# Kernel optimization log

Hardware: AMD Instinct MI355X
Metric: run time of the kernel (lower is better)

Reference implementation:

```python
import jax, jax.numpy as jnp
import numpy as np

B, IN, H, Z = 2048, 1024, 1024, 256


def setup_inputs() -> dict:
    key = jax.random.key(0)
    ks = jax.random.split(key, 17)
    s = 1.0 / np.sqrt(H)  # matches reset_parameters uniform(-stdv, stdv)
    u = lambda k, shape: jax.random.uniform(k, shape, minval=-s, maxval=s, dtype=jnp.float32)
    return {
        'src_x': jax.random.normal(ks[0], (B, IN), dtype=jnp.float32),
        'h': jax.random.normal(ks[1], (B, H), dtype=jnp.float32),
        'c': jax.random.normal(ks[2], (B, H), dtype=jnp.float32),
        'src_meta': jax.random.normal(ks[3], (B, Z), dtype=jnp.float32),
        'zh_w': u(ks[4], (4 * Z, Z)),
        'zh_b': u(ks[5], (4 * Z,)),
        'zx_w': u(ks[6], (4 * Z, Z)),
        'zx_b': u(ks[7], (4 * Z,)),
        'zb_w': u(ks[8], (4 * Z, Z)),
        'dh_w': u(ks[9], (4, H, Z)),
        'dx_w': u(ks[10], (4, H, Z)),
        'db_w': u(ks[11], (4, H, Z)),
        'db_b': u(ks[12], (4, H)),
        'w_h': u(ks[13], (4, H, H)),
        'w_x': u(ks[14], (4, H, IN)),
        'ln_w': u(ks[15], (4, H)),
        'ln_b': u(ks[16], (4, H)),
    }


def reference(src_x, h, c, src_meta, zh_w, zh_b, zx_w, zx_b, zb_w,
              dh_w, dx_w, db_w, db_b, w_h, w_x, ln_w, ln_b):
    b = src_x.shape[0]
    # hypernetwork projections, reshaped to [B, 4 gates, Z]
    zh = (src_meta @ zh_w.T + zh_b).reshape(b, 4, -1)
    zx = (src_meta @ zx_w.T + zx_b).reshape(b, 4, -1)
    zb = (src_meta @ zb_w.T).reshape(b, 4, -1)
    # per-gate scaling vectors d_h, d_x and bias d_b: [B, 4, H]
    d_h = jnp.einsum('bgz,ghz->bgh', zh, dh_w)
    d_x = jnp.einsum('bgz,ghz->bgh', zx, dx_w)
    d_b = jnp.einsum('bgz,ghz->bgh', zb, db_w) + db_b[None]
    # main LSTM matmuls: [B, 4, H]
    wh = jnp.einsum('ghj,bj->bgh', w_h, h)
    wx = jnp.einsum('ghj,bj->bgh', w_x, src_x)
    y = d_h * wh + d_x * wx + d_b
    # per-gate LayerNorm over hidden dim (eps = 1e-5, torch default)
    mu = jnp.mean(y, axis=-1, keepdims=True)
    var = jnp.var(y, axis=-1, keepdims=True)
    yn = (y - mu) * jax.lax.rsqrt(var + 1e-5) * ln_w[None] + ln_b[None]
    i, f, g, o = yn[:, 0], yn[:, 1], yn[:, 2], yn[:, 3]
    c_next = jax.nn.sigmoid(f) * c + jax.nn.sigmoid(i) * jnp.tanh(g)
    h_next = jax.nn.sigmoid(o) * jnp.tanh(c_next)
    return (h_next, c_next)
```

## Files before the change

kernel.cpp:

```cpp
#include <hip/hip_runtime.h>

typedef __attribute__((ext_vector_type(4))) float f32x4;
typedef __attribute__((ext_vector_type(16))) float f32x16;
typedef __attribute__((ext_vector_type(8))) short bf16x8;

#define DEVFN static __device__ __forceinline__

DEVFN unsigned short f2bf(float f) {
  union { float f; unsigned u; } x; x.f = f;
  unsigned r = x.u + 0x7fffu + ((x.u >> 16) & 1u);
  return (unsigned short)(r >> 16);
}
DEVFN float bf2f(unsigned short u) {
  union { unsigned u; float f; } x; x.u = ((unsigned)u) << 16;
  return x.f;
}

DEVFN void gload_lds16(const unsigned short* g, unsigned short* l) {
  __builtin_amdgcn_global_load_lds(
      (const __attribute__((address_space(1))) unsigned int*)g,
      (__attribute__((address_space(3))) unsigned int*)l, 16, 0, 0);
}

#define NSEG 8
struct SegTable {
  const float* src[NSEG];
  unsigned short* dst[NSEG];
  int chunks[NSEG];
};

__global__ __launch_bounds__(256) void cast_f32_bf16(SegTable st) {
  int c = blockIdx.x;
  int s = 0;
  while (c >= st.chunks[s]) { c -= st.chunks[s]; ++s; }
  const float* src = st.src[s] + (long)c * 4096;
  unsigned short* dst = st.dst[s] + (long)c * 4096;
  const int t = threadIdx.x;
#pragma unroll
  for (int i = 0; i < 4; ++i) {
    float4 v = *(const float4*)(src + t * 4 + i * 1024);
    ushort4 o;
    o.x = f2bf(v.x); o.y = f2bf(v.y); o.z = f2bf(v.z); o.w = f2bf(v.w);
    *(ushort4*)(dst + t * 4 + i * 1024) = o;
  }
}

__global__ __launch_bounds__(256) void tcast_z(
    const float* __restrict__ zh_w, const float* __restrict__ zx_w,
    const float* __restrict__ zb_w, unsigned short* __restrict__ WzT) {
  const int zz = blockIdx.z;
  const int t = zz >> 2, g = zz & 3;
  const float* src =
      (t == 0 ? zh_w : (t == 1 ? zx_w : zb_w)) + (long)g * 65536;
  unsigned short* dst = WzT + (long)zz * 65536;
  const int j0 = blockIdx.x * 64, k0 = blockIdx.y * 64;
  __shared__ float T[64][65];
  const int tid = threadIdx.x;
  const int jr = tid >> 2, kc = (tid & 3) * 16;
#pragma unroll
  for (int i = 0; i < 4; ++i) {
    float4 v = *(const float4*)(src + (long)(j0 + jr) * 256 + k0 + kc + i * 4);
    T[jr][kc + i * 4 + 0] = v.x;
    T[jr][kc + i * 4 + 1] = v.y;
    T[jr][kc + i * 4 + 2] = v.z;
    T[jr][kc + i * 4 + 3] = v.w;
  }
  __syncthreads();
  const int kr = tid >> 2, jc = (tid & 3) * 16;
  unsigned short tmp[16];
#pragma unroll
  for (int i = 0; i < 16; ++i) tmp[i] = f2bf(T[jc + i][kr]);
  *(bf16x8*)(dst + (long)(k0 + kr) * 256 + j0 + jc) = *(bf16x8*)&tmp[0];
  *(bf16x8*)(dst + (long)(k0 + kr) * 256 + j0 + jc + 8) = *(bf16x8*)&tmp[8];
}

__global__ __launch_bounds__(256) void fbias_kernel(
    const float* __restrict__ zh_b, const float* __restrict__ zx_b,
    const float* __restrict__ db_b, const float* __restrict__ dh_w,
    const float* __restrict__ dx_w, float* __restrict__ F) {
  if (blockIdx.x >= 128) {
    const int idx = (blockIdx.x - 128) * 1024 + threadIdx.x * 4;
    *(float4*)(F + 8192 + idx) = *(const float4*)(db_b + idx);
    return;
  }
  const int wgid = blockIdx.x * 4 + (threadIdx.x >> 6);
  const int lane = threadIdx.x & 63;
  const int t = wgid >> 8, g = (wgid >> 6) & 3, hbase = (wgid & 63) * 16;
  const float* zb = (t == 0 ? zh_b : zx_b) + g * 256;
  const float* dw = (t == 0 ? dh_w : dx_w) + (long)g * 262144;
  float4 zv = *(const float4*)(zb + lane * 4);
#pragma unroll
  for (int i = 0; i < 16; ++i) {
    const int h = hbase + i;
    float4 wv = *(const float4*)(dw + (long)h * 256 + lane * 4);
    float s = zv.x * wv.x + zv.y * wv.y + zv.z * wv.z + zv.w * wv.w;
#pragma unroll
    for (int off = 32; off; off >>= 1) s += __shfl_down(s, off);
    if (lane == 0) F[(t * 4 + g) * 1024 + h] = s;
  }
}

DEVFN void gemm128_body(const unsigned short* __restrict__ A,
                        const unsigned short* __restrict__ W,
                        unsigned short* __restrict__ C,
                        const float* __restrict__ bias,
                        int lda, int ldb, int ldc, int K,
                        int bx, int by,
                        unsigned short* As, unsigned short* Bs) {
  const int m0 = by * 128, n0 = bx * 128;
  const int tid = threadIdx.x;
  const int lane = tid & 63, wid = tid >> 6;
  const int wr = wid >> 1, wc = wid & 1;

  const int srow = tid >> 2, scol = (tid & 3) * 8;
  const unsigned short* Ag0 = A + (long)(m0 + srow) * lda + scol;
  const unsigned short* Ag1 = A + (long)(m0 + 64 + srow) * lda + scol;
  const unsigned short* Wg0 = W + (long)(n0 + srow) * ldb + scol;
  const unsigned short* Wg1 = W + (long)(n0 + 64 + srow) * ldb + scol;
  unsigned short* As0 = &As[tid * 8];
  unsigned short* As1 = &As[2048 + tid * 8];
  unsigned short* Bs0 = &Bs[tid * 8];
  unsigned short* Bs1 = &Bs[2048 + tid * 8];

  const int r = lane & 15, q = lane >> 4;

  f32x4 acc[4][4];
#pragma unroll
  for (int m = 0; m < 4; ++m)
#pragma unroll
    for (int n = 0; n < 4; ++n) acc[m][n] = (f32x4)0.f;

  for (int k0 = 0; k0 < K; k0 += 32) {
    gload_lds16(Ag0 + k0, As0);
    gload_lds16(Ag1 + k0, As1);
    gload_lds16(Wg0 + k0, Bs0);
    gload_lds16(Wg1 + k0, Bs1);
    __syncthreads();

    bf16x8 af[4], bfr[4];
#pragma unroll
    for (int m = 0; m < 4; ++m)
      af[m] = *(const bf16x8*)&As[(wr * 64 + m * 16 + r) * 32 + q * 8];
#pragma unroll
    for (int n = 0; n < 4; ++n)
      bfr[n] = *(const bf16x8*)&Bs[(wc * 64 + n * 16 + r) * 32 + q * 8];
#pragma unroll
    for (int m = 0; m < 4; ++m)
#pragma unroll
      for (int n = 0; n < 4; ++n)
        acc[m][n] = __builtin_amdgcn_mfma_f32_16x16x32_bf16(af[m], bfr[n],
                                                            acc[m][n], 0, 0, 0);
    __syncthreads();
  }

#pragma unroll
  for (int m = 0; m < 4; ++m) {
    const int row = m0 + wr * 64 + m * 16 + q * 4;
#pragma unroll
    for (int n = 0; n < 4; ++n) {
      const int col = n0 + wc * 64 + n * 16 + r;
      float bv = bias ? bias[col] : 0.f;
#pragma unroll
      for (int j = 0; j < 4; ++j) {
        float v = acc[m][n][j] + bv;
        C[(long)(row + j) * ldc + col] = f2bf(v);
      }
    }
  }
}

__global__ __launch_bounds__(256) void gemm_e(
    const unsigned short* __restrict__ Wd, const unsigned short* __restrict__ WzT,
    unsigned short* __restrict__ E) {
  __shared__ __align__(16) unsigned short As[4096];
  __shared__ __align__(16) unsigned short Bs[4096];
  const int zz = blockIdx.z;
  gemm128_body(Wd + (long)zz * 262144, WzT + (long)zz * 65536,
               E + (long)zz * 262144, nullptr,
               256, 256, 256, 256, blockIdx.x, blockIdx.y, As, Bs);
}

__global__ __launch_bounds__(256) void gemm_d(
    const unsigned short* __restrict__ meta_bf, const unsigned short* __restrict__ E,
    unsigned short* __restrict__ dall, const float* __restrict__ F) {
  __shared__ __align__(16) unsigned short As[4096];
  __shared__ __align__(16) unsigned short Bs[4096];
  const int zz = blockIdx.z;
  unsigned short* C = dall + (long)(zz >> 2) * 8388608 + (zz & 3) * 1024;
  gemm128_body(meta_bf, E + (long)zz * 262144, C, F + zz * 1024,
               256, 256, 4096, 256, blockIdx.x, blockIdx.y, As, Bs);
}

__global__ __launch_bounds__(512, 2) void gemm256_whx(
    const unsigned short* __restrict__ Aall,
    const unsigned short* __restrict__ Ball,
    unsigned short* __restrict__ Call) {
  __shared__ __align__(16) unsigned short As[2][2][8192];
  __shared__ __align__(16) unsigned short Bs[2][2][8192];

  const int bid = blockIdx.x;
  const int swz = (bid & 7) * 32 + (bid >> 3);
  const int z = swz >> 7;
  const int rr = swz & 127;
  const int sb = rr >> 5, wq = rr & 31;
  const int my = (sb & 1) * 4 + (wq >> 3);
  const int nx = (sb >> 1) * 8 + (wq & 7);

  const unsigned short* Ag = Aall + (long)z * 2097152 + (long)my * 262144;
  const unsigned short* Bg = Ball + (long)z * 4194304 + (long)nx * 262144;
  unsigned short* Cg = Call + (long)z * 8388608 + (long)my * 1048576 + nx * 256;

  const int tid = threadIdx.x;
  const int lane = tid & 63, wid = tid >> 6;
  const int wm = wid >> 2, wn = wid & 3;
  const int l31 = lane & 31, l5 = lane >> 5;
  const int sw = l31 & 7;

  const int srow = tid >> 3, sslot = tid & 7;
  const int gcol = (sslot ^ (srow & 7)) * 8;
  const unsigned short* AgS = Ag + (long)srow * 1024 + gcol;
  const unsigned short* BgS = Bg + (long)srow * 1024 + gcol;

  auto stageA = [&](int buf, int half, int kt) {
    const unsigned short* s = AgS + half * 131072 + kt * 64;
    unsigned short* d = &As[buf][half][tid * 8];
    gload_lds16(s, d);
    gload_lds16(s + 65536, d + 4096);
  };
  auto stageB = [&](int buf, int half, int kt) {
    const unsigned short* s = BgS + half * 131072 + kt * 64;
    unsigned short* d = &Bs[buf][half][tid * 8];
    gload_lds16(s, d);
    gload_lds16(s + 65536, d + 4096);
  };

  int koff[4];
#pragma unroll
  for (int ks = 0; ks < 4; ++ks) koff[ks] = ((ks * 2 + l5) ^ sw) * 8;

  const int bhalf = wn >> 1;
  int brow[2];
#pragma unroll
  for (int nt = 0; nt < 2; ++nt) brow[nt] = ((wn & 1) * 64 + nt * 32 + l31) * 64;
  int arow[4];
#pragma unroll
  for (int mt = 0; mt < 4; ++mt) arow[mt] = (mt * 32 + l31) * 64;

  f32x16 acc[4][2];
#pragma unroll
  for (int m = 0; m < 4; ++m)
#pragma unroll
    for (int n = 0; n < 2; ++n) acc[m][n] = (f32x16)0.f;

  stageA(0, 0, 0); stageB(0, 0, 0); stageA(0, 1, 0); stageB(0, 1, 0);
  stageA(1, 0, 1); stageB(1, 0, 1);
  asm volatile("s_waitcnt vmcnt(4)" ::: "memory");
  __builtin_amdgcn_s_barrier();

#pragma unroll 2
  for (int T = 0; T < 16; ++T) {
    const int buf = T & 1, nb = buf ^ 1;

    if (T < 15) { stageA(nb, 1, T + 1); stageB(nb, 1, T + 1); }

    bf16x8 bfg[2][4], af[2][4];
    const unsigned short* Ab = &As[buf][wm][0];
    {
      const unsigned short* Bb = &Bs[buf][bhalf][0];
#pragma unroll
      for (int nt = 0; nt < 2; ++nt)
#pragma unroll
        for (int ks = 0; ks < 4; ++ks)
          bfg[nt][ks] = *(const bf16x8*)(Bb + brow[nt] + koff[ks]);
#pragma unroll
      for (int m2 = 0; m2 < 2; ++m2)
#pragma unroll
        for (int ks = 0; ks < 4; ++ks)
          af[m2][ks] = *(const bf16x8*)(Ab + arow[m2] + koff[ks]);
    }

    __builtin_amdgcn_s_setprio(1);
#pragma unroll
    for (int m2 = 0; m2 < 2; ++m2)
#pragma unroll
      for (int nt = 0; nt < 2; ++nt)
#pragma unroll
        for (int ks = 0; ks < 4; ++ks)
          acc[m2][nt] = __builtin_amdgcn_mfma_f32_32x32x16_bf16(
              af[m2][ks], bfg[nt][ks], acc[m2][nt], 0, 0, 0);
    __builtin_amdgcn_s_setprio(0);

#pragma unroll
    for (int m2 = 0; m2 < 2; ++m2)
#pragma unroll
      for (int ks = 0; ks < 4; ++ks)
        af[m2][ks] = *(const bf16x8*)(Ab + arow[2 + m2] + koff[ks]);

    asm volatile("s_waitcnt lgkmcnt(0)" ::: "memory");
    __builtin_amdgcn_sched_barrier(0);
    __builtin_amdgcn_s_barrier();

    if (T < 14) { stageA(buf, 0, T + 2); stageB(buf, 0, T + 2); }

    __builtin_amdgcn_s_setprio(1);
#pragma unroll
    for (int m2 = 0; m2 < 2; ++m2)
#pragma unroll
      for (int nt = 0; nt < 2; ++nt)
#pragma unroll
        for (int ks = 0; ks < 4; ++ks)
          acc[2 + m2][nt] = __builtin_amdgcn_mfma_f32_32x32x16_bf16(
              af[m2][ks], bfg[nt][ks], acc[2 + m2][nt], 0, 0, 0);
    __builtin_amdgcn_s_setprio(0);

    if (T < 14) {
      asm volatile("s_waitcnt vmcnt(4)" ::: "memory");
      __builtin_amdgcn_s_barrier();
    } else if (T == 14) {
      asm volatile("s_waitcnt vmcnt(0)" ::: "memory");
      __builtin_amdgcn_s_barrier();
    }
  }

#pragma unroll
  for (int mt = 0; mt < 4; ++mt) {
#pragma unroll
    for (int nt = 0; nt < 2; ++nt) {
      const int rb = wm * 128 + mt * 32 + 4 * l5;
      const int cb = wn * 64 + nt * 32 + l31;
#pragma unroll
      for (int reg = 0; reg < 16; ++reg) {
        const int row = rb + (reg & 3) + 8 * (reg >> 2);
        Cg[(long)row * 4096 + cb] = f2bf(acc[mt][nt][reg]);
      }
    }
  }
}

DEVFN void ld4bf(const unsigned short* p, float* o) {
  ushort4 v = *(const ushort4*)p;
  o[0] = bf2f(v.x); o[1] = bf2f(v.y); o[2] = bf2f(v.z); o[3] = bf2f(v.w);
}

__global__ __launch_bounds__(256) void epilogue_kernel(
    const unsigned short* __restrict__ d_all,
    const unsigned short* __restrict__ whx,
    const float* __restrict__ c_in,
    const float* __restrict__ ln_w, const float* __restrict__ ln_b,
    float* __restrict__ out) {
  const long b = blockIdx.x;
  const int t = threadIdx.x;
  const int lane = t & 63, wid = t >> 6;

  const unsigned short* dh = d_all + b * 4096;
  const unsigned short* dx = d_all + 8388608L + b * 4096;
  const unsigned short* db = d_all + 16777216L + b * 4096;
  const unsigned short* wh = whx + b * 4096;
  const unsigned short* wx = whx + 8388608L + b * 4096;

  __shared__ float redS[4][4], redQ[4][4];
  float y[4][4];

#pragma unroll
  for (int g = 0; g < 4; ++g) {
    const int base = g * 1024 + t * 4;
    float fdh[4], fdx[4], fdb[4], fwh[4], fwx[4];
    ld4bf(dh + base, fdh);
    ld4bf(dx + base, fdx);
    ld4bf(db + base, fdb);
    ld4bf(wh + base, fwh);
    ld4bf(wx + base, fwx);
    float s = 0.f, sq = 0.f;
#pragma unroll
    for (int j = 0; j < 4; ++j) {
      float v = fdh[j] * fwh[j] + fdx[j] * fwx[j] + fdb[j];
      y[g][j] = v;
      s += v;
      sq += v * v;
    }
#pragma unroll
    for (int off = 32; off; off >>= 1) {
      s += __shfl_down(s, off);
      sq += __shfl_down(sq, off);
    }
    if (lane == 0) { redS[g][wid] = s; redQ[g][wid] = sq; }
  }
  __syncthreads();

  float yn[4][4];
#pragma unroll
  for (int g = 0; g < 4; ++g) {
    float S = redS[g][0] + redS[g][1] + redS[g][2] + redS[g][3];
    float SQ = redQ[g][0] + redQ[g][1] + redQ[g][2] + redQ[g][3];
    float mu = S * (1.f / 1024.f);
    float var = SQ * (1.f / 1024.f) - mu * mu;
    float rs = rsqrtf(var + 1e-5f);
    const int base = g * 1024 + t * 4;
    float4 lw = *(const float4*)(ln_w + base);
    float4 lb = *(const float4*)(ln_b + base);
    yn[g][0] = (y[g][0] - mu) * rs * lw.x + lb.x;
    yn[g][1] = (y[g][1] - mu) * rs * lw.y + lb.y;
    yn[g][2] = (y[g][2] - mu) * rs * lw.z + lb.z;
    yn[g][3] = (y[g][3] - mu) * rs * lw.w + lb.w;
  }

  float4 cp = *(const float4*)(c_in + b * 1024 + t * 4);
  float cin[4] = {cp.x, cp.y, cp.z, cp.w};
  float hn[4], cn[4];
#pragma unroll
  for (int j = 0; j < 4; ++j) {
    float ii = yn[0][j], ff = yn[1][j], gg = yn[2][j], oo = yn[3][j];
    float si = 1.f / (1.f + expf(-ii));
    float sf = 1.f / (1.f + expf(-ff));
    float so = 1.f / (1.f + expf(-oo));
    float cnj = sf * cin[j] + si * tanhf(gg);
    cn[j] = cnj;
    hn[j] = so * tanhf(cnj);
  }
  float4 ho = {hn[0], hn[1], hn[2], hn[3]};
  float4 co = {cn[0], cn[1], cn[2], cn[3]};
  *(float4*)(out + b * 1024 + t * 4) = ho;
  *(float4*)(out + 2097152L + b * 1024 + t * 4) = co;
}

extern "C" void kernel_launch(void* const* d_in, const int* in_sizes, int n_in,
                              void* d_out, int out_size, void* d_ws,
                              size_t ws_size, hipStream_t stream) {
  const float* src_x = (const float*)d_in[0];
  const float* h_in  = (const float*)d_in[1];
  const float* c_in  = (const float*)d_in[2];
  const float* meta  = (const float*)d_in[3];
  const float* zh_w  = (const float*)d_in[4];
  const float* zh_b  = (const float*)d_in[5];
  const float* zx_w  = (const float*)d_in[6];
  const float* zx_b  = (const float*)d_in[7];
  const float* zb_w  = (const float*)d_in[8];
  const float* dh_w  = (const float*)d_in[9];
  const float* dx_w  = (const float*)d_in[10];
  const float* db_w  = (const float*)d_in[11];
  const float* db_b  = (const float*)d_in[12];
  const float* w_h   = (const float*)d_in[13];
  const float* w_x   = (const float*)d_in[14];
  const float* ln_w  = (const float*)d_in[15];
  const float* ln_b  = (const float*)d_in[16];

  char* ws = (char*)d_ws;
  unsigned short* h_bf    = (unsigned short*)(ws + 0);
  unsigned short* x_bf    = (unsigned short*)(ws + 4194304);
  unsigned short* meta_bf = (unsigned short*)(ws + 8388608);
  unsigned short* Wh      = (unsigned short*)(ws + 9437184);
  unsigned short* Wx      = (unsigned short*)(ws + 17825792);
  unsigned short* Wd      = (unsigned short*)(ws + 26214400);
  unsigned short* WzT     = (unsigned short*)(ws + 32505856);
  unsigned short* E       = (unsigned short*)(ws + 34078720);
  float*          F       = (float*)(ws + 40370176);
  unsigned short* dall    = (unsigned short*)(ws + 40419328);
  unsigned short* whx     = (unsigned short*)(ws + 90750976);
  if (ws_size < 124305408) return;

  SegTable st;
  int i = 0, total = 0;
  auto add = [&](const float* s, unsigned short* d, int n) {
    st.src[i] = s; st.dst[i] = d; st.chunks[i] = n / 4096;
    total += n / 4096; ++i;
  };
  add(h_in, h_bf, 2048 * 1024);
  add(src_x, x_bf, 2048 * 1024);
  add(meta, meta_bf, 2048 * 256);
  add(w_h, Wh, 4096 * 1024);
  add(w_x, Wx, 4096 * 1024);
  add(dh_w, Wd, 4 * 1024 * 256);
  add(dx_w, Wd + 1048576, 4 * 1024 * 256);
  add(db_w, Wd + 2097152, 4 * 1024 * 256);
  cast_f32_bf16<<<total, 256, 0, stream>>>(st);

  tcast_z<<<dim3(4, 4, 12), 256, 0, stream>>>(zh_w, zx_w, zb_w, WzT);
  fbias_kernel<<<132, 256, 0, stream>>>(zh_b, zx_b, db_b, dh_w, dx_w, F);

  gemm_e<<<dim3(2, 8, 12), 256, 0, stream>>>(Wd, WzT, E);

  gemm_d<<<dim3(8, 16, 12), 256, 0, stream>>>(meta_bf, E, dall, F);

  gemm256_whx<<<256, 512, 0, stream>>>(h_bf, Wh, whx);

  epilogue_kernel<<<2048, 256, 0, stream>>>(dall, whx, c_in, ln_w, ln_b,
                                            (float*)d_out);
}
```

Measured before the change: 121.9 us.

## Fuse d_h/d_x/d_b hypernet GEMM with gating multiply into single Y kernel

Replaces the gemm_d kernel, which wrote the three d_h/d_x/d_b tensors to global memory, with gemm_y. For each gate tile, gemm_y computes all three projections in sequence, multiplies them by the wh/wx results read from whx, and writes a single combined pre-norm Y buffer. The epilogue then reads one bf16 tensor instead of five. This removes the d_all write and its read-back, but the whx reads in gemm_y are scattered per element (stride 4096), and the GEMM now runs after gemm256_whx instead of independently of it.

Result: slower. 128.3 us (+5.3%).

```diff
diff --git a/kernel.cpp b/kernel.cpp
--- a/kernel.cpp
+++ b/kernel.cpp
@@ -180,15 +180,112 @@
                256, 256, 256, 256, blockIdx.x, blockIdx.y, As, Bs);
 }
 
-__global__ __launch_bounds__(256) void gemm_d(
-    const unsigned short* __restrict__ meta_bf, const unsigned short* __restrict__ E,
-    unsigned short* __restrict__ dall, const float* __restrict__ F) {
+__global__ __launch_bounds__(256) void gemm_y(
+    const unsigned short* __restrict__ meta_bf,
+    const unsigned short* __restrict__ E,
+    const unsigned short* __restrict__ whx,
+    const float* __restrict__ F,
+    unsigned short* __restrict__ Y) {
   __shared__ __align__(16) unsigned short As[4096];
   __shared__ __align__(16) unsigned short Bs[4096];
-  const int zz = blockIdx.z;
-  unsigned short* C = dall + (long)(zz >> 2) * 8388608 + (zz & 3) * 1024;
-  gemm128_body(meta_bf, E + (long)zz * 262144, C, F + zz * 1024,
-               256, 256, 4096, 256, blockIdx.x, blockIdx.y, As, Bs);
+  const int g = blockIdx.z;
+  const int m0 = blockIdx.y * 128, n0 = blockIdx.x * 128;
+  const int tid = threadIdx.x;
+  const int lane = tid & 63, wid = tid >> 6;
+  const int wr = wid >> 1, wc = wid & 1;
+  const int r = lane & 15, q = lane >> 4;
+  const int srow = tid >> 2, scol = (tid & 3) * 8;
+
+  const unsigned short* Ag0 = meta_bf + (long)(m0 + srow) * 256 + scol;
+  const unsigned short* Ag1 = meta_bf + (long)(m0 + 64 + srow) * 256 + scol;
+  unsigned short* As0 = &As[tid * 8];
+  unsigned short* As1 = &As[2048 + tid * 8];
+  unsigned short* Bs0 = &Bs[tid * 8];
+  unsigned short* Bs1 = &Bs[2048 + tid * 8];
+
+  f32x4 yacc[4][4];
+#pragma unroll
+  for (int m = 0; m < 4; ++m)
+#pragma unroll
+    for (int n = 0; n < 4; ++n) yacc[m][n] = (f32x4)0.f;
+
+#pragma unroll 1
+  for (int t = 0; t < 3; ++t) {
+    const unsigned short* W = E + ((long)(t * 4 + g)) * 262144;
+    const unsigned short* Wg0 = W + (long)(n0 + srow) * 256 + scol;
+    const unsigned short* Wg1 = W + (long)(n0 + 64 + srow) * 256 + scol;
+
+    f32x4 acc[4][4];
+#pragma unroll
+    for (int m = 0; m < 4; ++m)
+#pragma unroll
+      for (int n = 0; n < 4; ++n) acc[m][n] = (f32x4)0.f;
+
+    for (int k0 = 0; k0 < 256; k0 += 32) {
+      gload_lds16(Ag0 + k0, As0);
+      gload_lds16(Ag1 + k0, As1);
+      gload_lds16(Wg0 + k0, Bs0);
+      gload_lds16(Wg1 + k0, Bs1);
+      __syncthreads();
+
+      bf16x8 af[4], bfr[4];
+#pragma unroll
+      for (int m = 0; m < 4; ++m)
+        af[m] = *(const bf16x8*)&As[(wr * 64 + m * 16 + r) * 32 + q * 8];
+#pragma unroll
+      for (int n = 0; n < 4; ++n)
+        bfr[n] = *(const bf16x8*)&Bs[(wc * 64 + n * 16 + r) * 32 + q * 8];
+#pragma unroll
+      for (int m = 0; m < 4; ++m)
+#pragma unroll
+        for (int n = 0; n < 4; ++n)
+          acc[m][n] = __builtin_amdgcn_mfma_f32_16x16x32_bf16(
+              af[m], bfr[n], acc[m][n], 0, 0, 0);
+      __syncthreads();
+    }
+
+    if (t < 2) {
+      const unsigned short* wsrc = whx + (long)t * 8388608;
+#pragma unroll
+      for (int n = 0; n < 4; ++n) {
+        const int cl = wc * 64 + n * 16 + r;
+        const float fv = F[(t * 4 + g) * 1024 + n0 + cl];
+        const long colg = (long)g * 1024 + n0 + cl;
+#pragma unroll
+        for (int m = 0; m < 4; ++m) {
+          const int row = m0 + wr * 64 + m * 16 + q * 4;
+#pragma unroll
+          for (int j = 0; j < 4; ++j) {
+            const float wv = bf2f(wsrc[(long)(row + j) * 4096 + colg]);
+            yacc[m][n][j] += (acc[m][n][j] + fv) * wv;
+          }
+        }
+      }
+    } else {
+#pragma unroll
+      for (int n = 0; n < 4; ++n) {
+        const int cl = wc * 64 + n * 16 + r;
+        const float fv = F[(8 + g) * 1024 + n0 + cl];
+#pragma unroll
+        for (int m = 0; m < 4; ++m)
+#pragma unroll
+          for (int j = 0; j < 4; ++j)
+            yacc[m][n][j] += acc[m][n][j] + fv;
+      }
+    }
+  }
+
+#pragma unroll
+  for (int m = 0; m < 4; ++m) {
+    const int row = m0 + wr * 64 + m * 16 + q * 4;
+#pragma unroll
+    for (int n = 0; n < 4; ++n) {
+      const long colg = (long)g * 1024 + n0 + wc * 64 + n * 16 + r;
+#pragma unroll
+      for (int j = 0; j < 4; ++j)
+        Y[(long)(row + j) * 4096 + colg] = f2bf(yacc[m][n][j]);
+    }
+  }
 }
 
 __global__ __launch_bounds__(512, 2) void gemm256_whx(
@@ -342,9 +439,8 @@
   o[0] = bf2f(v.x); o[1] = bf2f(v.y); o[2] = bf2f(v.z); o[3] = bf2f(v.w);
 }
 
-__global__ __launch_bounds__(256) void epilogue_kernel(
-    const unsigned short* __restrict__ d_all,
-    const unsigned short* __restrict__ whx,
+__global__ __launch_bounds__(256) void epilogue2(
+    const unsigned short* __restrict__ Y,
     const float* __restrict__ c_in,
     const float* __restrict__ ln_w, const float* __restrict__ ln_b,
     float* __restrict__ out) {
@@ -352,32 +448,15 @@
   const int t = threadIdx.x;
   const int lane = t & 63, wid = t >> 6;
 
-  const unsigned short* dh = d_all + b * 4096;
-  const unsigned short* dx = d_all + 8388608L + b * 4096;
-  const unsigned short* db = d_all + 16777216L + b * 4096;
-  const unsigned short* wh = whx + b * 4096;
-  const unsigned short* wx = whx + 8388608L + b * 4096;
-
   __shared__ float redS[4][4], redQ[4][4];
   float y[4][4];
 
 #pragma unroll
   for (int g = 0; g < 4; ++g) {
-    const int base = g * 1024 + t * 4;
-    float fdh[4], fdx[4], fdb[4], fwh[4], fwx[4];
-    ld4bf(dh + base, fdh);
-    ld4bf(dx + base, fdx);
-    ld4bf(db + base, fdb);
-    ld4bf(wh + base, fwh);
-    ld4bf(wx + base, fwx);
+    ld4bf(Y + b * 4096 + g * 1024 + t * 4, y[g]);
     float s = 0.f, sq = 0.f;
 #pragma unroll
-    for (int j = 0; j < 4; ++j) {
-      float v = fdh[j] * fwh[j] + fdx[j] * fwx[j] + fdb[j];
-      y[g][j] = v;
-      s += v;
-      sq += v * v;
-    }
+    for (int j = 0; j < 4; ++j) { s += y[g][j]; sq += y[g][j] * y[g][j]; }
 #pragma unroll
     for (int off = 32; off; off >>= 1) {
       s += __shfl_down(s, off);
@@ -454,9 +533,9 @@
   unsigned short* WzT     = (unsigned short*)(ws + 32505856);
   unsigned short* E       = (unsigned short*)(ws + 34078720);
   float*          F       = (float*)(ws + 40370176);
-  unsigned short* dall    = (unsigned short*)(ws + 40419328);
-  unsigned short* whx     = (unsigned short*)(ws + 90750976);
-  if (ws_size < 124305408) return;
+  unsigned short* Ybuf    = (unsigned short*)(ws + 40419328);
+  unsigned short* whx     = (unsigned short*)(ws + 57196544);
+  if (ws_size < 90750976) return;
 
   SegTable st;
   int i = 0, total = 0;
@@ -479,10 +558,9 @@
 
   gemm_e<<<dim3(2, 8, 12), 256, 0, stream>>>(Wd, WzT, E);
 
-  gemm_d<<<dim3(8, 16, 12), 256, 0, stream>>>(meta_bf, E, dall, F);
-
   gemm256_whx<<<256, 512, 0, stream>>>(h_bf, Wh, whx);
 
-  epilogue_kernel<<<2048, 256, 0, stream>>>(dall, whx, c_in, ln_w, ln_b,
-                                            (float*)d_out);
-}
+  gemm_y<<<dim3(8, 16, 4), 256, 0, stream>>>(meta_bf, E, whx, F, Ybuf);
+
+  epilogue2<<<2048, 256, 0, stream>>>(Ybuf, c_in, ln_w, ln_b, (float*)d_out);
+}
```

## Merge prep kernels into one launch and re-layout GEMM LDS tiles

Applied to the files above, without the earlier changes.

Folds the three small preprocessing kernels (f32-to-bf16 cast, Z-weight transpose-cast, bias fold) into a single prep_kernel that dispatches on block index, removing two launches and the gaps between them. Separately changes the LDS staging layout in gemm128_body and the 256-tile GEMM. Consecutive LDS segments now hold 8 rows by 8 k-elements instead of whole rows, which replaces the XOR swizzle with a blocked layout meant to cut bank conflicts on MFMA fragment reads. The new global-load addressing may coalesce differently, and the blocked layout may itself conflict.

Result: slower. 137.4 us (+12.7%).

```diff
diff --git a/kernel.cpp b/kernel.cpp
--- a/kernel.cpp
+++ b/kernel.cpp
@@ -29,62 +29,67 @@
   int chunks[NSEG];
 };
 
-__global__ __launch_bounds__(256) void cast_f32_bf16(SegTable st) {
-  int c = blockIdx.x;
-  int s = 0;
-  while (c >= st.chunks[s]) { c -= st.chunks[s]; ++s; }
-  const float* src = st.src[s] + (long)c * 4096;
-  unsigned short* dst = st.dst[s] + (long)c * 4096;
-  const int t = threadIdx.x;
-#pragma unroll
-  for (int i = 0; i < 4; ++i) {
-    float4 v = *(const float4*)(src + t * 4 + i * 1024);
-    ushort4 o;
-    o.x = f2bf(v.x); o.y = f2bf(v.y); o.z = f2bf(v.z); o.w = f2bf(v.w);
-    *(ushort4*)(dst + t * 4 + i * 1024) = o;
-  }
-}
-
-__global__ __launch_bounds__(256) void tcast_z(
+__global__ __launch_bounds__(256) void prep_kernel(
+    SegTable st, int castChunks,
     const float* __restrict__ zh_w, const float* __restrict__ zx_w,
-    const float* __restrict__ zb_w, unsigned short* __restrict__ WzT) {
-  const int zz = blockIdx.z;
-  const int t = zz >> 2, g = zz & 3;
-  const float* src =
-      (t == 0 ? zh_w : (t == 1 ? zx_w : zb_w)) + (long)g * 65536;
-  unsigned short* dst = WzT + (long)zz * 65536;
-  const int j0 = blockIdx.x * 64, k0 = blockIdx.y * 64;
-  __shared__ float T[64][65];
-  const int tid = threadIdx.x;
-  const int jr = tid >> 2, kc = (tid & 3) * 16;
-#pragma unroll
-  for (int i = 0; i < 4; ++i) {
-    float4 v = *(const float4*)(src + (long)(j0 + jr) * 256 + k0 + kc + i * 4);
-    T[jr][kc + i * 4 + 0] = v.x;
-    T[jr][kc + i * 4 + 1] = v.y;
-    T[jr][kc + i * 4 + 2] = v.z;
-    T[jr][kc + i * 4 + 3] = v.w;
-  }
-  __syncthreads();
-  const int kr = tid >> 2, jc = (tid & 3) * 16;
-  unsigned short tmp[16];
-#pragma unroll
-  for (int i = 0; i < 16; ++i) tmp[i] = f2bf(T[jc + i][kr]);
-  *(bf16x8*)(dst + (long)(k0 + kr) * 256 + j0 + jc) = *(bf16x8*)&tmp[0];
-  *(bf16x8*)(dst + (long)(k0 + kr) * 256 + j0 + jc + 8) = *(bf16x8*)&tmp[8];
-}
-
-__global__ __launch_bounds__(256) void fbias_kernel(
+    const float* __restrict__ zb_w, unsigned short* __restrict__ WzT,
     const float* __restrict__ zh_b, const float* __restrict__ zx_b,
     const float* __restrict__ db_b, const float* __restrict__ dh_w,
     const float* __restrict__ dx_w, float* __restrict__ F) {
-  if (blockIdx.x >= 128) {
-    const int idx = (blockIdx.x - 128) * 1024 + threadIdx.x * 4;
+  __shared__ float T[64][65];
+  const int tid = threadIdx.x;
+  int b = blockIdx.x;
+
+  if (b < castChunks) {
+    int c = b, s = 0;
+    while (c >= st.chunks[s]) { c -= st.chunks[s]; ++s; }
+    const float* src = st.src[s] + (long)c * 4096;
+    unsigned short* dst = st.dst[s] + (long)c * 4096;
+#pragma unroll
+    for (int i = 0; i < 4; ++i) {
+      float4 v = *(const float4*)(src + tid * 4 + i * 1024);
+      ushort4 o;
+      o.x = f2bf(v.x); o.y = f2bf(v.y); o.z = f2bf(v.z); o.w = f2bf(v.w);
+      *(ushort4*)(dst + tid * 4 + i * 1024) = o;
+    }
+    return;
+  }
+  b -= castChunks;
+
+  if (b < 192) {
+    const int zz = b >> 4, rem = b & 15;
+    const int t = zz >> 2, g = zz & 3;
+    const float* src =
+        (t == 0 ? zh_w : (t == 1 ? zx_w : zb_w)) + (long)g * 65536;
+    unsigned short* dst = WzT + (long)zz * 65536;
+    const int j0 = (rem & 3) * 64, k0 = (rem >> 2) * 64;
+    const int jr = tid >> 2, kc = (tid & 3) * 16;
+#pragma unroll
+    for (int i = 0; i < 4; ++i) {
+      float4 v = *(const float4*)(src + (long)(j0 + jr) * 256 + k0 + kc + i * 4);
+      T[jr][kc + i * 4 + 0] = v.x;
+      T[jr][kc + i * 4 + 1] = v.y;
+      T[jr][kc + i * 4 + 2] = v.z;
+      T[jr][kc + i * 4 + 3] = v.w;
+    }
+    __syncthreads();
+    const int kr = tid >> 2, jc = (tid & 3) * 16;
+    unsigned short tmp[16];
+#pragma unroll
+    for (int i = 0; i < 16; ++i) tmp[i] = f2bf(T[jc + i][kr]);
+    *(bf16x8*)(dst + (long)(k0 + kr) * 256 + j0 + jc) = *(bf16x8*)&tmp[0];
+    *(bf16x8*)(dst + (long)(k0 + kr) * 256 + j0 + jc + 8) = *(bf16x8*)&tmp[8];
+    return;
+  }
+  b -= 192;
+
+  if (b >= 128) {
+    const int idx = (b - 128) * 1024 + tid * 4;
     *(float4*)(F + 8192 + idx) = *(const float4*)(db_b + idx);
     return;
   }
-  const int wgid = blockIdx.x * 4 + (threadIdx.x >> 6);
-  const int lane = threadIdx.x & 63;
+  const int wgid = b * 4 + (tid >> 6);
+  const int lane = tid & 63;
   const int t = wgid >> 8, g = (wgid >> 6) & 3, hbase = (wgid & 63) * 16;
   const float* zb = (t == 0 ? zh_b : zx_b) + g * 256;
   const float* dw = (t == 0 ? dh_w : dx_w) + (long)g * 262144;
@@ -112,7 +117,8 @@
   const int lane = tid & 63, wid = tid >> 6;
   const int wr = wid >> 1, wc = wid & 1;
 
-  const int srow = tid >> 2, scol = (tid & 3) * 8;
+  const int srow = (tid >> 5) * 8 + (tid & 7);
+  const int scol = ((tid >> 3) & 3) * 8;
   const unsigned short* Ag0 = A + (long)(m0 + srow) * lda + scol;
   const unsigned short* Ag1 = A + (long)(m0 + 64 + srow) * lda + scol;
   const unsigned short* Wg0 = W + (long)(n0 + srow) * ldb + scol;
@@ -140,10 +146,12 @@
     bf16x8 af[4], bfr[4];
 #pragma unroll
     for (int m = 0; m < 4; ++m)
-      af[m] = *(const bf16x8*)&As[(wr * 64 + m * 16 + r) * 32 + q * 8];
+      af[m] = *(const bf16x8*)&As[(wr * 8 + m * 2 + (r >> 3)) * 256 +
+                                  (r & 7) * 8 + q * 64];
 #pragma unroll
     for (int n = 0; n < 4; ++n)
-      bfr[n] = *(const bf16x8*)&Bs[(wc * 64 + n * 16 + r) * 32 + q * 8];
+      bfr[n] = *(const bf16x8*)&Bs[(wc * 8 + n * 2 + (r >> 3)) * 256 +
+                                   (r & 7) * 8 + q * 64];
 #pragma unroll
     for (int m = 0; m < 4; ++m)
 #pragma unroll
@@ -155,7 +163,7 @@
 
 #pragma unroll
   for (int m = 0; m < 4; ++m) {
-    const int row = m0 + wr * 64 + m * 16 + q * 4;
+    const int row = m0 + wr * 64 + m * 16 + (lane >> 4) * 4;
 #pragma unroll
     for (int n = 0; n < 4; ++n) {
       const int col = n0 + wc * 64 + n * 16 + r;
@@ -214,10 +222,9 @@
   const int lane = tid & 63, wid = tid >> 6;
   const int wm = wid >> 2, wn = wid & 3;
   const int l31 = lane & 31, l5 = lane >> 5;
-  const int sw = l31 & 7;
-
-  const int srow = tid >> 3, sslot = tid & 7;
-  const int gcol = (sslot ^ (srow & 7)) * 8;
+
+  const int srow = (tid >> 6) * 8 + (tid & 7);
+  const int gcol = ((tid >> 3) & 7) * 8;
   const unsigned short* AgS = Ag + (long)srow * 1024 + gcol;
   const unsigned short* BgS = Bg + (long)srow * 1024 + gcol;
 
@@ -236,15 +243,17 @@
 
   int koff[4];
 #pragma unroll
-  for (int ks = 0; ks < 4; ++ks) koff[ks] = ((ks * 2 + l5) ^ sw) * 8;
+  for (int ks = 0; ks < 4; ++ks) koff[ks] = (ks * 2 + l5) * 64;
 
   const int bhalf = wn >> 1;
   int brow[2];
 #pragma unroll
-  for (int nt = 0; nt < 2; ++nt) brow[nt] = ((wn & 1) * 64 + nt * 32 + l31) * 64;
+  for (int nt = 0; nt < 2; ++nt)
+    brow[nt] = ((wn & 1) * 8 + nt * 4 + (l31 >> 3)) * 512 + (l31 & 7) * 8;
   int arow[4];
 #pragma unroll
-  for (int mt = 0; mt < 4; ++mt) arow[mt] = (mt * 32 + l31) * 64;
+  for (int mt = 0; mt < 4; ++mt)
+    arow[mt] = (mt * 4 + (l31 >> 3)) * 512 + (l31 & 7) * 8;
 
   f32x16 acc[4][2];
 #pragma unroll
@@ -472,10 +481,9 @@
   add(dh_w, Wd, 4 * 1024 * 256);
   add(dx_w, Wd + 1048576, 4 * 1024 * 256);
   add(db_w, Wd + 2097152, 4 * 1024 * 256);
-  cast_f32_bf16<<<total, 256, 0, stream>>>(st);
-
-  tcast_z<<<dim3(4, 4, 12), 256, 0, stream>>>(zh_w, zx_w, zb_w, WzT);
-  fbias_kernel<<<132, 256, 0, stream>>>(zh_b, zx_b, db_b, dh_w, dx_w, F);
+
+  prep_kernel<<<total + 192 + 132, 256, 0, stream>>>(
+      st, total, zh_w, zx_w, zb_w, WzT, zh_b, zx_b, db_b, dh_w, dx_w, F);
 
   gemm_e<<<dim3(2, 8, 12), 256, 0, stream>>>(Wd, WzT, E);
 
```
